# Optimization experiments

Hardware: AMD Instinct MI355X
Metric: run time of the kernel (lower is better)

The kernel has to match this reference:

```python
import jax, jax.numpy as jnp
import numpy as np

HEADS = 4
HEAD_DIM = 32
SCALE = HEAD_DIM ** (-0.5)


def setup_inputs() -> dict:
    key = jax.random.key(0)
    k1, k2, k3, k4 = jax.random.split(key, 4)
    x = jax.random.normal(k1, (32, 256, 64, 64), dtype=jnp.float32)
    # to_qkv: Conv2d(256 -> 3*heads*head_dim=384, kernel 1x1, bias=False)
    w_qkv = jax.random.normal(k2, (384, 256), dtype=jnp.float32) * 0.02
    # to_out: Conv2d(128 -> 256, kernel 1x1, bias=True)
    w_out = jax.random.normal(k3, (256, 128), dtype=jnp.float32) * 0.02
    b_out = jax.random.normal(k4, (256,), dtype=jnp.float32) * 0.02
    return {"x": x, "w_qkv": w_qkv, "w_out": w_out, "b_out": b_out}


def reference(x, w_qkv, w_out, b_out):
    b, c, H, W = x.shape
    n = H * W
    # 1x1 conv == channel matmul; produce (b, 3, heads, head_dim, n)
    qkv = jnp.einsum('oc,bchw->bohw', w_qkv, x).reshape(b, 3, HEADS, HEAD_DIM, n)
    q, k, v = qkv[:, 0], qkv[:, 1], qkv[:, 2]  # each (b, h, d, n)
    q = jax.nn.softmax(q, axis=-1) * SCALE     # softmax over spatial n
    k = jax.nn.softmax(k, axis=-2)             # softmax over channel d
    # context: (b, h, e, d) -- reduce over n
    context = jnp.einsum('bhen,bhdn->bhed', k, v)
    # out: (b, h, d, n)
    out = jnp.einsum('bhed,bhen->bhdn', context, q)
    out = out.reshape(b, HEADS * HEAD_DIM, H, W)
    # to_out 1x1 conv with bias
    return jnp.einsum('oc,bchw->bohw', w_out, out) + b_out[None, :, None, None]
```

## Files before the change

### kernel.cpp

```cpp
#include <hip/hip_runtime.h>
#include <hip/hip_bf16.h>

#define NTOK 4096
#define SCALE 0.17677669529663687f

#define SWZ(r) ((((r) >> 1) ^ ((r) >> 3)) & 3)

using f32x4 = __attribute__((ext_vector_type(4))) float;
using s16x8 = __attribute__((ext_vector_type(8))) short;

__device__ __forceinline__ ushort bf_rne(float f) {
  unsigned int u = __builtin_bit_cast(unsigned int, f);
  u += 0x7FFFu + ((u >> 16) & 1u);
  return (ushort)(u >> 16);
}
__device__ __forceinline__ unsigned int pk2(float a, float b) {
  __hip_bfloat162 h = __float22bfloat162_rn(make_float2(a, b));
  unsigned int u;
  __builtin_memcpy(&u, &h, 4);
  return u;
}
__device__ __forceinline__ void gl_lds16(const ushort* g, ushort* l) {
  __builtin_amdgcn_global_load_lds(
      (const __attribute__((address_space(1))) unsigned int*)g,
      (__attribute__((address_space(3))) unsigned int*)l, 16, 0, 0);
}

__global__ __launch_bounds__(256) void k_cvt_w(const float* __restrict__ w,
                                               ushort* __restrict__ wb) {
  const int i = blockIdx.x * 256 + threadIdx.x;
  const float4 v = reinterpret_cast<const float4*>(w)[i];
  ushort4 h;
  h.x = bf_rne(v.x); h.y = bf_rne(v.y); h.z = bf_rne(v.z); h.w = bf_rne(v.w);
  reinterpret_cast<ushort4*>(wb)[i] = h;
}

__global__ __launch_bounds__(256) void k_qkv_mfma(const float* __restrict__ x,
                                                  const ushort* __restrict__ wb,
                                                  ushort* __restrict__ Ecn,
                                                  ushort* __restrict__ kb,
                                                  ushort* __restrict__ vb,
                                                  float* __restrict__ spart) {
  const int n0 = blockIdx.x * 128;
  const int o0 = blockIdx.y * 128;
  const int b  = blockIdx.z;
  const float* xb = x + (size_t)b * 256 * NTOK;

  __shared__ ushort As[4096];
  __shared__ ushort Bs[4096];

  const int t = threadIdx.x;
  const int lane = t & 63;
  const int wv = t >> 6;
  const int wr = wv >> 1, wc = wv & 1;
  const int lm = lane & 15;
  const int lk = lane >> 4;

  int aoff[4], boff[4];
#pragma unroll
  for (int mf = 0; mf < 4; ++mf) {
    const int ar = wr * 64 + mf * 16 + lm;
    aoff[mf] = ar * 32 + 8 * (lk ^ SWZ(ar));
  }
#pragma unroll
  for (int nf = 0; nf < 4; ++nf) {
    const int br = wc * 64 + nf * 16 + lm;
    boff[nf] = br * 32 + 8 * (lk ^ SWZ(br));
  }
  const int s1 = t, s2 = t + 256;
  const int r1 = s1 >> 2, q1 = (s1 & 3) ^ SWZ(r1);
  const int r2 = s2 >> 2, q2 = (s2 & 3) ^ SWZ(r2);
  const size_t ga1 = (size_t)(o0 + r1) * 256 + q1 * 8;
  const size_t ga2 = (size_t)(o0 + r2) * 256 + q2 * 8;
  const int lbase1 = wv * 512;
  const int lbase2 = 2048 + wv * 512;
  int sst[2], sn[2], sco[2];
#pragma unroll
  for (int i = 0; i < 2; ++i) {
    const int u = t + 256 * i;
    sn[i] = u & 127;
    sco[i] = u >> 7;
    sst[i] = sn[i] * 32 + 8 * (sco[i] ^ SWZ(sn[i]));
  }

  f32x4 acc[4][4];
#pragma unroll
  for (int i = 0; i < 4; ++i)
#pragma unroll
    for (int j = 0; j < 4; ++j) acc[i][j] = (f32x4){0.f, 0.f, 0.f, 0.f};

  float pre[16];
#pragma unroll
  for (int i = 0; i < 2; ++i)
#pragma unroll
    for (int j = 0; j < 8; ++j)
      pre[i * 8 + j] = xb[(size_t)(sco[i] * 8 + j) * NTOK + n0 + sn[i]];

  for (int it = 0; it < 8; ++it) {
    const size_t c0 = (size_t)it * 32;
    gl_lds16(wb + ga1 + c0, As + lbase1);
    gl_lds16(wb + ga2 + c0, As + lbase2);
#pragma unroll
    for (int i = 0; i < 2; ++i) {
      union { s16x8 v; unsigned int u[4]; } pk;
      pk.u[0] = pk2(pre[i * 8 + 0], pre[i * 8 + 1]);
      pk.u[1] = pk2(pre[i * 8 + 2], pre[i * 8 + 3]);
      pk.u[2] = pk2(pre[i * 8 + 4], pre[i * 8 + 5]);
      pk.u[3] = pk2(pre[i * 8 + 6], pre[i * 8 + 7]);
      *reinterpret_cast<s16x8*>(Bs + sst[i]) = pk.v;
    }
    __syncthreads();
    if (it < 7) {
      const size_t c1 = c0 + 32;
#pragma unroll
      for (int i = 0; i < 2; ++i)
#pragma unroll
        for (int j = 0; j < 8; ++j)
          pre[i * 8 + j] = xb[(c1 + sco[i] * 8 + j) * NTOK + n0 + sn[i]];
    }
    s16x8 af[4], bf[4];
#pragma unroll
    for (int mf = 0; mf < 4; ++mf)
      af[mf] = *reinterpret_cast<const s16x8*>(As + aoff[mf]);
#pragma unroll
    for (int nf = 0; nf < 4; ++nf)
      bf[nf] = *reinterpret_cast<const s16x8*>(Bs + boff[nf]);
#pragma unroll
    for (int mf = 0; mf < 4; ++mf)
#pragma unroll
      for (int nf = 0; nf < 4; ++nf)
        acc[mf][nf] = __builtin_amdgcn_mfma_f32_16x16x32_bf16(af[mf], bf[nf], acc[mf][nf], 0, 0, 0);
    __syncthreads();
  }

  if (blockIdx.y == 0) {
    ushort* C = Ecn + (size_t)b * 128 * NTOK + n0;
    float* sp = spart + (((size_t)b * 32 + blockIdx.x) * 2 + wc) * 128;
#pragma unroll
    for (int mf = 0; mf < 4; ++mf) {
#pragma unroll
      for (int r = 0; r < 4; ++r) {
        const int ch = wr * 64 + mf * 16 + lk * 4 + r;
        float s = 0.f;
#pragma unroll
        for (int nf = 0; nf < 4; ++nf) {
          const float e = __expf(acc[mf][nf][r]);
          s += e;
          C[(size_t)ch * NTOK + wc * 64 + nf * 16 + lm] = bf_rne(e);
        }
        s += __shfl_xor(s, 1, 64);
        s += __shfl_xor(s, 2, 64);
        s += __shfl_xor(s, 4, 64);
        s += __shfl_xor(s, 8, 64);
        if (lm == 0) sp[ch] = s;
      }
    }
  } else if (blockIdx.y == 1) {
#pragma unroll
    for (int nf = 0; nf < 4; ++nf) {
#pragma unroll
      for (int g = 0; g < 2; ++g) {
        float m = -1e30f;
#pragma unroll
        for (int mm = 0; mm < 2; ++mm)
#pragma unroll
          for (int r = 0; r < 4; ++r)
            m = fmaxf(m, acc[g * 2 + mm][nf][r]);
        m = fmaxf(m, __shfl_xor(m, 16, 64));
        m = fmaxf(m, __shfl_xor(m, 32, 64));
        float s = 0.f;
#pragma unroll
        for (int mm = 0; mm < 2; ++mm)
#pragma unroll
          for (int r = 0; r < 4; ++r) {
            const float e = __expf(acc[g * 2 + mm][nf][r] - m);
            acc[g * 2 + mm][nf][r] = e;
            s += e;
          }
        s += __shfl_xor(s, 16, 64);
        s += __shfl_xor(s, 32, 64);
        const float inv = 1.0f / s;
#pragma unroll
        for (int mm = 0; mm < 2; ++mm)
#pragma unroll
          for (int r = 0; r < 4; ++r) acc[g * 2 + mm][nf][r] *= inv;
      }
    }
    ushort* C = kb + (size_t)b * 128 * NTOK + n0;
#pragma unroll
    for (int mf = 0; mf < 4; ++mf) {
      const int row0 = wr * 64 + mf * 16 + lk * 4;
#pragma unroll
      for (int nf = 0; nf < 4; ++nf) {
        const int col = wc * 64 + nf * 16 + lm;
#pragma unroll
        for (int r = 0; r < 4; ++r)
          C[(size_t)(row0 + r) * NTOK + col] = bf_rne(acc[mf][nf][r]);
      }
    }
  } else {
    ushort* C = vb + (size_t)b * 128 * NTOK + n0;
#pragma unroll
    for (int mf = 0; mf < 4; ++mf) {
      const int row0 = wr * 64 + mf * 16 + lk * 4;
#pragma unroll
      for (int nf = 0; nf < 4; ++nf) {
        const int col = wc * 64 + nf * 16 + lm;
#pragma unroll
        for (int r = 0; r < 4; ++r)
          C[(size_t)(row0 + r) * NTOK + col] = bf_rne(acc[mf][nf][r]);
      }
    }
  }
}

__global__ __launch_bounds__(256) void k_context_mfma(const ushort* __restrict__ kb,
                                                      const ushort* __restrict__ vb,
                                                      float* __restrict__ ctx_part) {
  const int bh = blockIdx.x;
  const int w = threadIdx.x >> 6;
  const int lane = threadIdx.x & 63;
  const int lm = lane & 15, lk = lane >> 4;
  const ushort* kp = kb + (size_t)bh * 32 * NTOK + (size_t)w * 1024;
  const ushort* vp = vb + (size_t)bh * 32 * NTOK + (size_t)w * 1024;
  f32x4 acc[2][2];
#pragma unroll
  for (int i = 0; i < 2; ++i)
#pragma unroll
    for (int j = 0; j < 2; ++j) acc[i][j] = (f32x4){0.f, 0.f, 0.f, 0.f};
#pragma unroll 4
  for (int ks = 0; ks < 32; ++ks) {
    const int coff = ks * 32 + lk * 8;
    const s16x8 a0 = *reinterpret_cast<const s16x8*>(kp + (size_t)lm * NTOK + coff);
    const s16x8 a1 = *reinterpret_cast<const s16x8*>(kp + (size_t)(16 + lm) * NTOK + coff);
    const s16x8 b0 = *reinterpret_cast<const s16x8*>(vp + (size_t)lm * NTOK + coff);
    const s16x8 b1 = *reinterpret_cast<const s16x8*>(vp + (size_t)(16 + lm) * NTOK + coff);
    acc[0][0] = __builtin_amdgcn_mfma_f32_16x16x32_bf16(a0, b0, acc[0][0], 0, 0, 0);
    acc[0][1] = __builtin_amdgcn_mfma_f32_16x16x32_bf16(a0, b1, acc[0][1], 0, 0, 0);
    acc[1][0] = __builtin_amdgcn_mfma_f32_16x16x32_bf16(a1, b0, acc[1][0], 0, 0, 0);
    acc[1][1] = __builtin_amdgcn_mfma_f32_16x16x32_bf16(a1, b1, acc[1][1], 0, 0, 0);
  }
  float* op = ctx_part + ((size_t)bh * 4 + w) * 1024;
#pragma unroll
  for (int et = 0; et < 2; ++et)
#pragma unroll
    for (int dt = 0; dt < 2; ++dt)
#pragma unroll
      for (int r = 0; r < 4; ++r)
        op[(et * 16 + lk * 4 + r) * 32 + dt * 16 + lm] = acc[et][dt][r];
}

__global__ __launch_bounds__(256) void k_w2(const float* __restrict__ ctx_part,
                                            const float* __restrict__ spart,
                                            const float* __restrict__ w_out,
                                            ushort* __restrict__ W2b) {
  const int b = blockIdx.x;
  const int t = threadIdx.x;
  __shared__ float ctx[4096];
  __shared__ float fbuf[128];
#pragma unroll
  for (int i = 0; i < 16; ++i) {
    const int idx = t + 256 * i;
    const int h = idx >> 10, ed = idx & 1023;
    const float* cp = ctx_part + ((size_t)((b * 4 + h) * 4)) * 1024 + ed;
    ctx[idx] = cp[0] + cp[1024] + cp[2048] + cp[3072];
  }
  if (t < 128) {
    float s = 0.f;
    for (int p = 0; p < 64; ++p) s += spart[((size_t)b * 64 + p) * 128 + t];
    fbuf[t] = SCALE / s;
  }
  __syncthreads();
  const float* wrow = w_out + (size_t)t * 128;
  ushort* wout_row = W2b + ((size_t)b * 256 + t) * 128;
  float wv[32];
  for (int h = 0; h < 4; ++h) {
#pragma unroll
    for (int d = 0; d < 32; ++d) wv[d] = wrow[h * 32 + d];
#pragma unroll 4
    for (int e = 0; e < 32; ++e) {
      float a = 0.f;
#pragma unroll
      for (int d = 0; d < 32; ++d) a += wv[d] * ctx[h * 1024 + e * 32 + d];
      wout_row[h * 32 + e] = bf_rne(a * fbuf[h * 32 + e]);
    }
  }
}

__global__ __launch_bounds__(256) void k_out_mfma(const ushort* __restrict__ Ecn,
                                                  const ushort* __restrict__ W2b,
                                                  const float* __restrict__ b_out,
                                                  float* __restrict__ out) {
  const int n0 = blockIdx.x * 128;
  const int o0 = blockIdx.y * 128;
  const int b  = blockIdx.z;
  const ushort* A  = W2b + (size_t)b * 256 * 128;
  const ushort* Bq = Ecn + (size_t)b * 128 * NTOK;

  __shared__ ushort As[8192];
  __shared__ ushort Bt[8192];

  const int t = threadIdx.x;
  const int lane = t & 63;
  const int wv = t >> 6;
  const int wr = wv >> 1, wc = wv & 1;
  const int lm = lane & 15;
  const int lk = lane >> 4;

  int aoff[4][2], boff[4][2];
#pragma unroll
  for (int mf = 0; mf < 4; ++mf) {
    const int ar = wr * 64 + mf * 16 + lm;
#pragma unroll
    for (int ks = 0; ks < 2; ++ks)
      aoff[mf][ks] = ar * 64 + 8 * ((ks * 4 + lk) ^ (ar & 7));
  }
#pragma unroll
  for (int nf = 0; nf < 4; ++nf) {
    const int br = wc * 64 + nf * 16 + lm;
#pragma unroll
    for (int ks = 0; ks < 2; ++ks)
      boff[nf][ks] = br * 64 + 8 * ((ks * 4 + lk) ^ (br & 7));
  }
  size_t gaA[4];
  int lb[4];
#pragma unroll
  for (int i = 0; i < 4; ++i) {
    const int s_total = t + 256 * i;
    const int r = s_total >> 3;
    const int q = (s_total & 7) ^ (r & 7);
    gaA[i] = (size_t)(o0 + r) * 128 + q * 8;
    lb[i] = wv * 512 + i * 2048;
  }
  int bst[8], bn[8], bcg[8];
#pragma unroll
  for (int i = 0; i < 8; ++i) {
    const int u = t + 256 * i;
    bn[i] = u & 127;
    bcg[i] = u >> 7;
    bst[i] = bn[i] * 64 + 8 * ((bcg[i] >> 1) ^ (bn[i] & 7)) + (bcg[i] & 1) * 4;
  }

  f32x4 acc[4][4];
#pragma unroll
  for (int i = 0; i < 4; ++i)
#pragma unroll
    for (int j = 0; j < 4; ++j) acc[i][j] = (f32x4){0.f, 0.f, 0.f, 0.f};

  for (int it = 0; it < 2; ++it) {
    const size_t c0 = (size_t)it * 64;
    __syncthreads();
#pragma unroll
    for (int i = 0; i < 4; ++i)
      gl_lds16(A + gaA[i] + c0, As + lb[i]);
#pragma unroll
    for (int i = 0; i < 8; ++i) {
      const ushort* gp = Bq + (c0 + bcg[i] * 4) * NTOK + n0 + bn[i];
      ushort4 hvec;
      hvec.x = gp[0];
      hvec.y = gp[NTOK];
      hvec.z = gp[2 * NTOK];
      hvec.w = gp[3 * NTOK];
      *reinterpret_cast<ushort4*>(Bt + bst[i]) = hvec;
    }
    __syncthreads();
#pragma unroll
    for (int ks = 0; ks < 2; ++ks) {
      s16x8 af[4], bf[4];
#pragma unroll
      for (int mf = 0; mf < 4; ++mf)
        af[mf] = *reinterpret_cast<const s16x8*>(As + aoff[mf][ks]);
#pragma unroll
      for (int nf = 0; nf < 4; ++nf)
        bf[nf] = *reinterpret_cast<const s16x8*>(Bt + boff[nf][ks]);
#pragma unroll
      for (int mf = 0; mf < 4; ++mf)
#pragma unroll
        for (int nf = 0; nf < 4; ++nf)
          acc[mf][nf] = __builtin_amdgcn_mfma_f32_16x16x32_bf16(af[mf], bf[nf], acc[mf][nf], 0, 0, 0);
    }
  }

  float* C = out + ((size_t)b * 256 + o0) * NTOK + n0;
#pragma unroll
  for (int mf = 0; mf < 4; ++mf) {
    const int row0 = wr * 64 + mf * 16 + lk * 4;
#pragma unroll
    for (int nf = 0; nf < 4; ++nf) {
      const int col = wc * 64 + nf * 16 + lm;
#pragma unroll
      for (int r = 0; r < 4; ++r) {
        const float bias = b_out[o0 + row0 + r];
        C[(size_t)(row0 + r) * NTOK + col] = acc[mf][nf][r] + bias;
      }
    }
  }
}

extern "C" void kernel_launch(void* const* d_in, const int* in_sizes, int n_in,
                              void* d_out, int out_size, void* d_ws, size_t ws_size,
                              hipStream_t stream) {
  const float* x     = (const float*)d_in[0];
  const float* w_qkv = (const float*)d_in[1];
  const float* w_out = (const float*)d_in[2];
  const float* b_out = (const float*)d_in[3];
  float* out = (float*)d_out;

  ushort* kb  = (ushort*)d_ws;
  ushort* vb  = kb + (size_t)16777216;
  ushort* Ecn = vb + (size_t)16777216;
  float*  ctx_part = (float*)(Ecn + (size_t)16777216);
  float*  spart    = ctx_part + 524288;
  ushort* wb  = (ushort*)(spart + 262144);
  ushort* W2b = wb + 98304;

  k_cvt_w<<<96, 256, 0, stream>>>(w_qkv, wb);
  k_qkv_mfma<<<dim3(32, 3, 32), 256, 0, stream>>>(x, wb, Ecn, kb, vb, spart);
  k_context_mfma<<<128, 256, 0, stream>>>(kb, vb, ctx_part);
  k_w2<<<32, 256, 0, stream>>>(ctx_part, spart, w_out, W2b);
  k_out_mfma<<<dim3(32, 2, 32), 256, 0, stream>>>(Ecn, W2b, b_out, out);
}
```

Before: 176.6 us.

## Load full x tile once into LDS and compute q,k,v in one block

The qkv projection kernel no longer launches three blocks per token tile (one each for q, k and v), each re-reading the same x slice. It now loads the whole 256-channel by 128-token x tile into LDS once as bf16 and loops over the three output groups inside a single block. Weight fragments are read straight from global memory (relying on cache) instead of being staged through LDS, and the per-k-step barriers are gone. This cuts x reads to a third, but it uses 64KB of LDS per block, which lowers occupancy, and there is no overlap between the x load and the MFMA work.

```diff
diff --git a/kernel.cpp b/kernel.cpp
--- a/kernel.cpp
+++ b/kernel.cpp
@@ -42,12 +42,10 @@
                                                   ushort* __restrict__ vb,
                                                   float* __restrict__ spart) {
   const int n0 = blockIdx.x * 128;
-  const int o0 = blockIdx.y * 128;
-  const int b  = blockIdx.z;
+  const int b  = blockIdx.y;
   const float* xb = x + (size_t)b * 256 * NTOK;
 
-  __shared__ ushort As[4096];
-  __shared__ ushort Bs[4096];
+  __shared__ ushort Bs[128 * 256];
 
   const int t = threadIdx.x;
   const int lane = t & 63;
@@ -56,159 +54,134 @@
   const int lm = lane & 15;
   const int lk = lane >> 4;
 
-  int aoff[4], boff[4];
-#pragma unroll
-  for (int mf = 0; mf < 4; ++mf) {
-    const int ar = wr * 64 + mf * 16 + lm;
-    aoff[mf] = ar * 32 + 8 * (lk ^ SWZ(ar));
-  }
-#pragma unroll
-  for (int nf = 0; nf < 4; ++nf) {
-    const int br = wc * 64 + nf * 16 + lm;
-    boff[nf] = br * 32 + 8 * (lk ^ SWZ(br));
-  }
-  const int s1 = t, s2 = t + 256;
-  const int r1 = s1 >> 2, q1 = (s1 & 3) ^ SWZ(r1);
-  const int r2 = s2 >> 2, q2 = (s2 & 3) ^ SWZ(r2);
-  const size_t ga1 = (size_t)(o0 + r1) * 256 + q1 * 8;
-  const size_t ga2 = (size_t)(o0 + r2) * 256 + q2 * 8;
-  const int lbase1 = wv * 512;
-  const int lbase2 = 2048 + wv * 512;
-  int sst[2], sn[2], sco[2];
-#pragma unroll
-  for (int i = 0; i < 2; ++i) {
+#pragma unroll
+  for (int i = 0; i < 16; ++i) {
     const int u = t + 256 * i;
-    sn[i] = u & 127;
-    sco[i] = u >> 7;
-    sst[i] = sn[i] * 32 + 8 * (sco[i] ^ SWZ(sn[i]));
-  }
-
-  f32x4 acc[4][4];
-#pragma unroll
-  for (int i = 0; i < 4; ++i)
-#pragma unroll
-    for (int j = 0; j < 4; ++j) acc[i][j] = (f32x4){0.f, 0.f, 0.f, 0.f};
-
-  float pre[16];
-#pragma unroll
-  for (int i = 0; i < 2; ++i)
-#pragma unroll
-    for (int j = 0; j < 8; ++j)
-      pre[i * 8 + j] = xb[(size_t)(sco[i] * 8 + j) * NTOK + n0 + sn[i]];
-
-  for (int it = 0; it < 8; ++it) {
-    const size_t c0 = (size_t)it * 32;
-    gl_lds16(wb + ga1 + c0, As + lbase1);
-    gl_lds16(wb + ga2 + c0, As + lbase2);
-#pragma unroll
-    for (int i = 0; i < 2; ++i) {
-      union { s16x8 v; unsigned int u[4]; } pk;
-      pk.u[0] = pk2(pre[i * 8 + 0], pre[i * 8 + 1]);
-      pk.u[1] = pk2(pre[i * 8 + 2], pre[i * 8 + 3]);
-      pk.u[2] = pk2(pre[i * 8 + 4], pre[i * 8 + 5]);
-      pk.u[3] = pk2(pre[i * 8 + 6], pre[i * 8 + 7]);
-      *reinterpret_cast<s16x8*>(Bs + sst[i]) = pk.v;
-    }
-    __syncthreads();
-    if (it < 7) {
-      const size_t c1 = c0 + 32;
-#pragma unroll
-      for (int i = 0; i < 2; ++i)
-#pragma unroll
-        for (int j = 0; j < 8; ++j)
-          pre[i * 8 + j] = xb[(c1 + sco[i] * 8 + j) * NTOK + n0 + sn[i]];
-    }
-    s16x8 af[4], bf[4];
+    const int n = u & 127;
+    const int coct = u >> 7;
+    const float* gp = xb + (size_t)(coct * 8) * NTOK + n0 + n;
+    union { s16x8 v; unsigned int w[4]; } pk;
+#pragma unroll
+    for (int j = 0; j < 4; ++j)
+      pk.w[j] = pk2(gp[(size_t)(2 * j) * NTOK], gp[(size_t)(2 * j + 1) * NTOK]);
+    *reinterpret_cast<s16x8*>(Bs + n * 256 + 8 * (coct ^ (n & 7))) = pk.v;
+  }
+  __syncthreads();
+
+  int brow[4];
+#pragma unroll
+  for (int nf = 0; nf < 4; ++nf) brow[nf] = wc * 64 + nf * 16 + lm;
+
+#pragma unroll
+  for (int y = 0; y < 3; ++y) {
+    const int o0 = y * 128;
+    const ushort* abase[4];
 #pragma unroll
     for (int mf = 0; mf < 4; ++mf)
-      af[mf] = *reinterpret_cast<const s16x8*>(As + aoff[mf]);
-#pragma unroll
-    for (int nf = 0; nf < 4; ++nf)
-      bf[nf] = *reinterpret_cast<const s16x8*>(Bs + boff[nf]);
-#pragma unroll
-    for (int mf = 0; mf < 4; ++mf)
-#pragma unroll
-      for (int nf = 0; nf < 4; ++nf)
-        acc[mf][nf] = __builtin_amdgcn_mfma_f32_16x16x32_bf16(af[mf], bf[nf], acc[mf][nf], 0, 0, 0);
-    __syncthreads();
-  }
-
-  if (blockIdx.y == 0) {
-    ushort* C = Ecn + (size_t)b * 128 * NTOK + n0;
-    float* sp = spart + (((size_t)b * 32 + blockIdx.x) * 2 + wc) * 128;
-#pragma unroll
-    for (int mf = 0; mf < 4; ++mf) {
-#pragma unroll
-      for (int r = 0; r < 4; ++r) {
-        const int ch = wr * 64 + mf * 16 + lk * 4 + r;
-        float s = 0.f;
+      abase[mf] = wb + (size_t)(o0 + wr * 64 + mf * 16 + lm) * 256 + lk * 8;
+
+    f32x4 acc[4][4];
+#pragma unroll
+    for (int i = 0; i < 4; ++i)
+#pragma unroll
+      for (int j = 0; j < 4; ++j) acc[i][j] = (f32x4){0.f, 0.f, 0.f, 0.f};
+
+#pragma unroll
+    for (int it = 0; it < 8; ++it) {
+      s16x8 af[4], bf[4];
+#pragma unroll
+      for (int mf = 0; mf < 4; ++mf)
+        af[mf] = *reinterpret_cast<const s16x8*>(abase[mf] + it * 32);
+#pragma unroll
+      for (int nf = 0; nf < 4; ++nf) {
+        const int cc = it * 4 + lk;
+        bf[nf] = *reinterpret_cast<const s16x8*>(
+            Bs + brow[nf] * 256 + 8 * (cc ^ (brow[nf] & 7)));
+      }
+#pragma unroll
+      for (int mf = 0; mf < 4; ++mf)
+#pragma unroll
+        for (int nf = 0; nf < 4; ++nf)
+          acc[mf][nf] = __builtin_amdgcn_mfma_f32_16x16x32_bf16(af[mf], bf[nf], acc[mf][nf], 0, 0, 0);
+    }
+
+    if (y == 0) {
+      ushort* C = Ecn + (size_t)b * 128 * NTOK + n0;
+      float* sp = spart + (((size_t)b * 32 + blockIdx.x) * 2 + wc) * 128;
+#pragma unroll
+      for (int mf = 0; mf < 4; ++mf) {
+#pragma unroll
+        for (int r = 0; r < 4; ++r) {
+          const int ch = wr * 64 + mf * 16 + lk * 4 + r;
+          float s = 0.f;
+#pragma unroll
+          for (int nf = 0; nf < 4; ++nf) {
+            const float e = __expf(acc[mf][nf][r]);
+            s += e;
+            C[(size_t)ch * NTOK + wc * 64 + nf * 16 + lm] = bf_rne(e);
+          }
+          s += __shfl_xor(s, 1, 64);
+          s += __shfl_xor(s, 2, 64);
+          s += __shfl_xor(s, 4, 64);
+          s += __shfl_xor(s, 8, 64);
+          if (lm == 0) sp[ch] = s;
+        }
+      }
+    } else if (y == 1) {
+#pragma unroll
+      for (int nf = 0; nf < 4; ++nf) {
+#pragma unroll
+        for (int g = 0; g < 2; ++g) {
+          float m = -1e30f;
+#pragma unroll
+          for (int mm = 0; mm < 2; ++mm)
+#pragma unroll
+            for (int r = 0; r < 4; ++r)
+              m = fmaxf(m, acc[g * 2 + mm][nf][r]);
+          m = fmaxf(m, __shfl_xor(m, 16, 64));
+          m = fmaxf(m, __shfl_xor(m, 32, 64));
+          float s = 0.f;
+#pragma unroll
+          for (int mm = 0; mm < 2; ++mm)
+#pragma unroll
+            for (int r = 0; r < 4; ++r) {
+              const float e = __expf(acc[g * 2 + mm][nf][r] - m);
+              acc[g * 2 + mm][nf][r] = e;
+              s += e;
+            }
+          s += __shfl_xor(s, 16, 64);
+          s += __shfl_xor(s, 32, 64);
+          const float inv = 1.0f / s;
+#pragma unroll
+          for (int mm = 0; mm < 2; ++mm)
+#pragma unroll
+            for (int r = 0; r < 4; ++r) acc[g * 2 + mm][nf][r] *= inv;
+        }
+      }
+      ushort* C = kb + (size_t)b * 128 * NTOK + n0;
+#pragma unroll
+      for (int mf = 0; mf < 4; ++mf) {
+        const int row0 = wr * 64 + mf * 16 + lk * 4;
 #pragma unroll
         for (int nf = 0; nf < 4; ++nf) {
-          const float e = __expf(acc[mf][nf][r]);
-          s += e;
-          C[(size_t)ch * NTOK + wc * 64 + nf * 16 + lm] = bf_rne(e);
+          const int col = wc * 64 + nf * 16 + lm;
+#pragma unroll
+          for (int r = 0; r < 4; ++r)
+            C[(size_t)(row0 + r) * NTOK + col] = bf_rne(acc[mf][nf][r]);
         }
-        s += __shfl_xor(s, 1, 64);
-        s += __shfl_xor(s, 2, 64);
-        s += __shfl_xor(s, 4, 64);
-        s += __shfl_xor(s, 8, 64);
-        if (lm == 0) sp[ch] = s;
-      }
-    }
-  } else if (blockIdx.y == 1) {
-#pragma unroll
-    for (int nf = 0; nf < 4; ++nf) {
-#pragma unroll
-      for (int g = 0; g < 2; ++g) {
-        float m = -1e30f;
-#pragma unroll
-        for (int mm = 0; mm < 2; ++mm)
+      }
+    } else {
+      ushort* C = vb + (size_t)b * 128 * NTOK + n0;
+#pragma unroll
+      for (int mf = 0; mf < 4; ++mf) {
+        const int row0 = wr * 64 + mf * 16 + lk * 4;
+#pragma unroll
+        for (int nf = 0; nf < 4; ++nf) {
+          const int col = wc * 64 + nf * 16 + lm;
 #pragma unroll
           for (int r = 0; r < 4; ++r)
-            m = fmaxf(m, acc[g * 2 + mm][nf][r]);
-        m = fmaxf(m, __shfl_xor(m, 16, 64));
-        m = fmaxf(m, __shfl_xor(m, 32, 64));
-        float s = 0.f;
-#pragma unroll
-        for (int mm = 0; mm < 2; ++mm)
-#pragma unroll
-          for (int r = 0; r < 4; ++r) {
-            const float e = __expf(acc[g * 2 + mm][nf][r] - m);
-            acc[g * 2 + mm][nf][r] = e;
-            s += e;
-          }
-        s += __shfl_xor(s, 16, 64);
-        s += __shfl_xor(s, 32, 64);
-        const float inv = 1.0f / s;
-#pragma unroll
-        for (int mm = 0; mm < 2; ++mm)
-#pragma unroll
-          for (int r = 0; r < 4; ++r) acc[g * 2 + mm][nf][r] *= inv;
-      }
-    }
-    ushort* C = kb + (size_t)b * 128 * NTOK + n0;
-#pragma unroll
-    for (int mf = 0; mf < 4; ++mf) {
-      const int row0 = wr * 64 + mf * 16 + lk * 4;
-#pragma unroll
-      for (int nf = 0; nf < 4; ++nf) {
-        const int col = wc * 64 + nf * 16 + lm;
-#pragma unroll
-        for (int r = 0; r < 4; ++r)
-          C[(size_t)(row0 + r) * NTOK + col] = bf_rne(acc[mf][nf][r]);
-      }
-    }
-  } else {
-    ushort* C = vb + (size_t)b * 128 * NTOK + n0;
-#pragma unroll
-    for (int mf = 0; mf < 4; ++mf) {
-      const int row0 = wr * 64 + mf * 16 + lk * 4;
-#pragma unroll
-      for (int nf = 0; nf < 4; ++nf) {
-        const int col = wc * 64 + nf * 16 + lm;
-#pragma unroll
-        for (int r = 0; r < 4; ++r)
-          C[(size_t)(row0 + r) * NTOK + col] = bf_rne(acc[mf][nf][r]);
+            C[(size_t)(row0 + r) * NTOK + col] = bf_rne(acc[mf][nf][r]);
+        }
       }
     }
   }
@@ -415,7 +388,7 @@
   ushort* W2b = wb + 98304;
 
   k_cvt_w<<<96, 256, 0, stream>>>(w_qkv, wb);
-  k_qkv_mfma<<<dim3(32, 3, 32), 256, 0, stream>>>(x, wb, Ecn, kb, vb, spart);
+  k_qkv_mfma<<<dim3(32, 32), 256, 0, stream>>>(x, wb, Ecn, kb, vb, spart);
   k_context_mfma<<<128, 256, 0, stream>>>(kb, vb, ctx_part);
   k_w2<<<32, 256, 0, stream>>>(ctx_part, spart, w_out, W2b);
   k_out_mfma<<<dim3(32, 2, 32), 256, 0, stream>>>(Ecn, W2b, b_out, out);
```

Result: no change. 180.0 us (+1.9%).
